# Optimization experiments

Measured on AMD Instinct MI355X. Metric: run time of the kernel, lower is better.

## Reference

```python
import jax, jax.numpy as jnp
import numpy as np

N_SAMPLE = 32
BETA = 1.0


def setup_inputs() -> dict:
    key = jax.random.key(0)
    k1, k2 = jax.random.split(key)
    # small scales so the gaussian kernel over 512 dims does not underflow
    x = jax.random.normal(k1, (2048, 512), dtype=jnp.float32) * 0.05
    W = jax.random.normal(k2, (512, 2048), dtype=jnp.float32) * 0.02  # Dense kernel [in, hidden]
    return {"x": x, "W": W}


def reference(x, W):
    B, H = x.shape[0], W.shape[1]
    # Encoder: h = x W ; z = softmax(h * beita)
    h = x @ W                                   # [B, H]
    z = jax.nn.softmax(h * BETA, axis=-1)       # [B, H]
    # Sampler: tf.random.categorical treats z (probs) as LOGITS -> same here.
    key = jax.random.key(42)
    # tf gives [B, n_sample]; jax categorical with shape=(NS, B) then .T matches that,
    # and the original code then RESHAPES (not transposes) to [NS, B] -> replicate scramble.
    samp = jax.random.categorical(key, z, axis=-1, shape=(N_SAMPLE, B)).T  # [B, NS]
    samp = samp.reshape(N_SAMPLE, B)            # faithful reshape, not transpose
    onehot = jax.nn.one_hot(samp, H, dtype=x.dtype)          # [NS, B, H]
    # tensordot(onehot, W, axes=[2,1]) -> gather rows of W^T as dense matmul
    x_decoded = jnp.einsum('nbh,dh->nbd', onehot, W)          # [NS, B, D]
    # gauss(x[None], x_decoded), var=1
    diff = x[None, :, :] - x_decoded                          # [NS, B, D]
    coeff = 1.0 / jnp.sqrt(2.0 * jnp.pi)
    temp = coeff * jnp.exp(-0.5 * jnp.sum(diff * diff, axis=-1))  # [NS, B]
    weight = temp / jnp.mean(temp, axis=0)                    # broadcast over NS
    return (h, z, onehot, x_decoded, weight)
```

## Files before the change

### kernel.cpp

```cpp
#include <hip/hip_runtime.h>
#include <stdint.h>
#include <math.h>

static constexpr int BDIM = 2048;
static constexpr int HDIM = 2048;
static constexpr int DDIM = 512;
static constexpr int NSAMP = 32;

static constexpr size_t OFF_H  = 0;
static constexpr size_t OFF_Z  = (size_t)BDIM * HDIM;
static constexpr size_t OFF_OH = OFF_Z + (size_t)BDIM * HDIM;
static constexpr size_t OFF_XD = OFF_OH + (size_t)NSAMP * BDIM * HDIM;
static constexpr size_t OFF_W  = OFF_XD + (size_t)NSAMP * BDIM * DDIM;

static constexpr size_t WS_WT    = 0;
static constexpr size_t WS_XB    = 1048576;
static constexpr size_t WS_WTB   = WS_XB + 524288;
static constexpr size_t WS_TEMP  = WS_WTB + 524288;
static constexpr size_t WS_DELTA = WS_TEMP + 65536;

typedef __attribute__((ext_vector_type(8))) short short8;
typedef __attribute__((ext_vector_type(4))) float f32x4;

__device__ __forceinline__ ushort f2bf(float f) {
  uint32_t x = __float_as_uint(f);
  return (ushort)((x + 0x7FFFu + ((x >> 16) & 1u)) >> 16);
}

__global__ __launch_bounds__(256) void cast_x_kernel(const float* __restrict__ x,
                                                     ushort* __restrict__ xb) {
  const int i = (blockIdx.x * 256 + threadIdx.x) * 4;
  float4 v = *(const float4*)(x + i);
  ushort4 o = {f2bf(v.x), f2bf(v.y), f2bf(v.z), f2bf(v.w)};
  *(ushort4*)(xb + i) = o;
}

__global__ __launch_bounds__(256) void transpose_kernel(const float* __restrict__ W,
                                                        float* __restrict__ Wt,
                                                        ushort* __restrict__ Wtb) {
  __shared__ float tile[32][33];
  const int tx = threadIdx.x & 31, ty = threadIdx.x >> 5;
  const int bx = blockIdx.x;
  const int by = blockIdx.y;
#pragma unroll
  for (int i = 0; i < 32; i += 8)
    tile[ty + i][tx] = W[(size_t)(by * 32 + ty + i) * HDIM + bx * 32 + tx];
  __syncthreads();
#pragma unroll
  for (int i = 0; i < 32; i += 8) {
    float v = tile[tx][ty + i];
    const size_t o = (size_t)(bx * 32 + ty + i) * DDIM + by * 32 + tx;
    Wt[o] = v;
    Wtb[o] = f2bf(v);
  }
}

__global__ __launch_bounds__(256) void gemm_mfma_kernel(const ushort* __restrict__ xb,
                                                        const ushort* __restrict__ wtb,
                                                        float* __restrict__ h) {
  __shared__ short As[128][72];
  __shared__ short Bs[128][72];
  const int tid = threadIdx.x;
  const int bm = blockIdx.y * 128, bn = blockIdx.x * 128;
  const int wave = tid >> 6, lane = tid & 63;
  const int wm = (wave >> 1) * 64, wn = (wave & 1) * 64;
  const int lrow = lane & 15, lk = (lane >> 4) * 8;

  f32x4 acc[4][4] = {};

  const int srow = tid >> 3;
  const int scol = (tid & 7) * 8;

  for (int k0 = 0; k0 < DDIM; k0 += 64) {
#pragma unroll
    for (int p = 0; p < 4; ++p) {
      const int r = srow + p * 32;
      short8 av = *(const short8*)(xb + (size_t)(bm + r) * DDIM + k0 + scol);
      short8 bv = *(const short8*)(wtb + (size_t)(bn + r) * DDIM + k0 + scol);
      *(short8*)&As[r][scol] = av;
      *(short8*)&Bs[r][scol] = bv;
    }
    __syncthreads();
#pragma unroll
    for (int kk = 0; kk < 64; kk += 32) {
      short8 af[4], bf[4];
#pragma unroll
      for (int i = 0; i < 4; ++i) {
        af[i] = *(const short8*)&As[wm + i * 16 + lrow][kk + lk];
        bf[i] = *(const short8*)&Bs[wn + i * 16 + lrow][kk + lk];
      }
#pragma unroll
      for (int i = 0; i < 4; ++i)
#pragma unroll
        for (int j = 0; j < 4; ++j)
          acc[i][j] = __builtin_amdgcn_mfma_f32_16x16x32_bf16(af[i], bf[j], acc[i][j], 0, 0, 0);
    }
    __syncthreads();
  }
#pragma unroll
  for (int i = 0; i < 4; ++i)
#pragma unroll
    for (int j = 0; j < 4; ++j)
#pragma unroll
      for (int rg = 0; rg < 4; ++rg) {
        const int row = bm + wm + i * 16 + (lane >> 4) * 4 + rg;
        const int col = bn + wn + j * 16 + (lane & 15);
        h[(size_t)row * HDIM + col] = acc[i][j][rg];
      }
}

__global__ __launch_bounds__(256) void softmax_kernel(const float* __restrict__ h,
                                                      float* __restrict__ z,
                                                      float* __restrict__ rowDelta) {
  const int b = blockIdx.x;
  const int tid = threadIdx.x;
  const int lane = tid & 63, wav = tid >> 6;
  const float* row = h + (size_t)b * HDIM;
  float* zrow = z + (size_t)b * HDIM;
  __shared__ float wmaxs[4], wmins[4], wsums[4];

  float vals[8];
  float vmax = -INFINITY, vmin = INFINITY;
#pragma unroll
  for (int k = 0; k < 8; ++k) {
    float v = row[tid + (k << 8)];
    vals[k] = v;
    vmax = fmaxf(vmax, v);
    vmin = fminf(vmin, v);
  }
#pragma unroll
  for (int off = 32; off > 0; off >>= 1) {
    vmax = fmaxf(vmax, __shfl_xor(vmax, off, 64));
    vmin = fminf(vmin, __shfl_xor(vmin, off, 64));
  }
  if (lane == 0) { wmaxs[wav] = vmax; wmins[wav] = vmin; }
  __syncthreads();
  const float rmax = fmaxf(fmaxf(wmaxs[0], wmaxs[1]), fmaxf(wmaxs[2], wmaxs[3]));
  const float rmin = fminf(fminf(wmins[0], wmins[1]), fminf(wmins[2], wmins[3]));

  float e[8];
  float lsum = 0.f;
#pragma unroll
  for (int k = 0; k < 8; ++k) {
    e[k] = expf(vals[k] - rmax);
    lsum += e[k];
  }
#pragma unroll
  for (int off = 32; off > 0; off >>= 1) lsum += __shfl_xor(lsum, off, 64);
  if (lane == 0) wsums[wav] = lsum;
  __syncthreads();
  const float rsum = wsums[0] + wsums[1] + wsums[2] + wsums[3];
#pragma unroll
  for (int k = 0; k < 8; ++k) zrow[tid + (k << 8)] = e[k] / rsum;
  if (tid == 0) rowDelta[b] = (1.0f - expf(rmin - rmax)) / rsum;
}

__device__ __forceinline__ void threefry_0_42(uint32_t x0, uint32_t x1,
                                              uint32_t& o0, uint32_t& o1) {
  const uint32_t ks0 = 0u, ks1 = 42u, ks2 = 0x1BD11BDAu ^ 0u ^ 42u;
  x0 += ks0; x1 += ks1;
#define TF_R(r) { x0 += x1; x1 = (x1 << (r)) | (x1 >> (32 - (r))); x1 ^= x0; }
  TF_R(13) TF_R(15) TF_R(26) TF_R(6)   x0 += ks1; x1 += ks2 + 1u;
  TF_R(17) TF_R(29) TF_R(16) TF_R(24)  x0 += ks2; x1 += ks0 + 2u;
  TF_R(13) TF_R(15) TF_R(26) TF_R(6)   x0 += ks0; x1 += ks1 + 3u;
  TF_R(17) TF_R(29) TF_R(16) TF_R(24)  x0 += ks1; x1 += ks2 + 4u;
  TF_R(13) TF_R(15) TF_R(26) TF_R(6)   x0 += ks2; x1 += ks0 + 5u;
#undef TF_R
  o0 = x0; o1 = x1;
}

__device__ __forceinline__ float bits_to_u(uint32_t bits) {
  float f = __uint_as_float((bits >> 9) | 0x3f800000u) - 1.0f;
  return (f == 0.0f) ? 1.1754943508222875e-38f : f;
}

__global__ __launch_bounds__(256) void sample_fused_kernel(
    const float* __restrict__ z, const float* __restrict__ rowDelta,
    const float* __restrict__ x, const float* __restrict__ Wt,
    float* __restrict__ oh, float* __restrict__ xd, float* __restrict__ temp) {
  const int wav = threadIdx.x >> 6;
  const int lane = threadIdx.x & 63;
  const int r = blockIdx.x * 4 + wav;
  const int b = r & (BDIM - 1);
  const float* zrow = z + (size_t)b * HDIM;

  const uint32_t base = (uint32_t)r << 11;
  uint32_t bb[32];
  uint32_t m23 = 0u;
#pragma unroll
  for (int k = 0; k < 32; ++k) {
    uint32_t o0, o1;
    threefry_0_42(0u, base + (uint32_t)(lane + (k << 6)), o0, o1);
    bb[k] = (o0 ^ o1) >> 9;
    m23 = max(m23, bb[k]);
  }
#pragma unroll
  for (int off = 32; off > 0; off >>= 1)
    m23 = max(m23, (uint32_t)__shfl_xor((int)m23, off, 64));
  const float umax = bits_to_u(m23 << 9);

  const float dpad = rowDelta[b] + 3e-4f;
  float uthr = expf(-expf(-(-logf(-logf(umax)) - dpad)));
  uthr = __uint_as_float(__float_as_uint(uthr) - 4u);
  uint32_t thr23 = __float_as_uint(1.0f + uthr) & 0x7FFFFFu;
  if (thr23 > 0u) thr23 -= 1u;

  double best = -1e300; int bh = 0x7fffffff;
#pragma unroll
  for (int k = 0; k < 32; ++k) {
    if (bb[k] >= thr23 || bb[k] == m23) {
      const int hh = lane + (k << 6);
      const float uk = bits_to_u(bb[k] << 9);
      double s = -log(-log((double)uk)) + (double)zrow[hh];
      if (s > best || (s == best && hh < bh)) { best = s; bh = hh; }
    }
  }
#pragma unroll
  for (int off = 32; off > 0; off >>= 1) {
    double so = __shfl_xor(best, off, 64);
    int ho = __shfl_xor(bh, off, 64);
    if (so > best || (so == best && ho < bh)) { best = so; bh = ho; }
  }

  const int j = ((r & (BDIM - 1)) << 5) | (r >> 11);
  const int c = j & (BDIM - 1);

  float* ohrow = oh + (size_t)j * HDIM;
#pragma unroll
  for (int k = 0; k < 8; ++k) {
    const int idx4 = (k << 6) + lane;
    const unsigned d = (unsigned)(bh - (idx4 << 2));
    float4 v;
    v.x = (d == 0u) ? 1.f : 0.f;
    v.y = (d == 1u) ? 1.f : 0.f;
    v.z = (d == 2u) ? 1.f : 0.f;
    v.w = (d == 3u) ? 1.f : 0.f;
    ((float4*)ohrow)[idx4] = v;
  }

  const float4* wrow = (const float4*)(Wt + (size_t)bh * DDIM);
  const float4* xrow = (const float4*)(x + (size_t)c * DDIM);
  float4* xdrow = (float4*)(xd + (size_t)j * DDIM);
  float ss = 0.f;
#pragma unroll
  for (int k = 0; k < 2; ++k) {
    const int idx4 = (k << 6) + lane;
    const float4 wv = wrow[idx4];
    const float4 xv = xrow[idx4];
    xdrow[idx4] = wv;
    const float dx = xv.x - wv.x, dy = xv.y - wv.y;
    const float dz = xv.z - wv.z, dw = xv.w - wv.w;
    ss += dx * dx + dy * dy + dz * dz + dw * dw;
  }
#pragma unroll
  for (int off = 32; off > 0; off >>= 1) ss += __shfl_xor(ss, off, 64);
  if (lane == 0) temp[j] = 0.3989422804014327f * expf(-0.5f * ss);
}

__global__ __launch_bounds__(256) void weight_kernel(const float* __restrict__ temp,
                                                     float* __restrict__ wout) {
  const int c = blockIdx.x * 256 + threadIdx.x;
  if (c >= BDIM) return;
  float sum = 0.f;
#pragma unroll
  for (int a = 0; a < NSAMP; ++a) sum += temp[a * BDIM + c];
  const float mean = sum / 32.0f;
#pragma unroll
  for (int a = 0; a < NSAMP; ++a) wout[a * BDIM + c] = temp[a * BDIM + c] / mean;
}

extern "C" void kernel_launch(void* const* d_in, const int* in_sizes, int n_in,
                              void* d_out, int out_size, void* d_ws, size_t ws_size,
                              hipStream_t stream) {
  (void)in_sizes; (void)n_in; (void)out_size; (void)ws_size;
  const float* x = (const float*)d_in[0];
  const float* W = (const float*)d_in[1];
  float* out = (float*)d_out;

  float* h  = out + OFF_H;
  float* z  = out + OFF_Z;
  float* oh = out + OFF_OH;
  float* xd = out + OFF_XD;
  float* wo = out + OFF_W;

  float* ws = (float*)d_ws;
  float* Wt = ws + WS_WT;
  ushort* xb = (ushort*)(ws + WS_XB);
  ushort* Wtb = (ushort*)(ws + WS_WTB);
  float* temp = ws + WS_TEMP;
  float* rowDelta = ws + WS_DELTA;

  cast_x_kernel<<<1024, 256, 0, stream>>>(x, xb);
  transpose_kernel<<<dim3(64, 16), 256, 0, stream>>>(W, Wt, Wtb);
  gemm_mfma_kernel<<<dim3(16, 16), 256, 0, stream>>>(xb, Wtb, h);
  softmax_kernel<<<2048, 256, 0, stream>>>(h, z, rowDelta);
  sample_fused_kernel<<<16384, 256, 0, stream>>>(z, rowDelta, x, Wt, oh, xd, temp);
  weight_kernel<<<8, 256, 0, stream>>>(temp, wo);
}
```

Baseline: 871.4 us.

## Merge prep kernels, vectorize softmax, nontemporal stores and early loads in sampler

```diff
diff --git a/kernel.cpp b/kernel.cpp
--- a/kernel.cpp
+++ b/kernel.cpp
@@ -27,21 +27,22 @@
   return (ushort)((x + 0x7FFFu + ((x >> 16) & 1u)) >> 16);
 }
 
-__global__ __launch_bounds__(256) void cast_x_kernel(const float* __restrict__ x,
-                                                     ushort* __restrict__ xb) {
-  const int i = (blockIdx.x * 256 + threadIdx.x) * 4;
-  float4 v = *(const float4*)(x + i);
-  ushort4 o = {f2bf(v.x), f2bf(v.y), f2bf(v.z), f2bf(v.w)};
-  *(ushort4*)(xb + i) = o;
-}
-
-__global__ __launch_bounds__(256) void transpose_kernel(const float* __restrict__ W,
-                                                        float* __restrict__ Wt,
-                                                        ushort* __restrict__ Wtb) {
+__global__ __launch_bounds__(256) void prep_kernel(const float* __restrict__ x,
+                                                   ushort* __restrict__ xb,
+                                                   const float* __restrict__ W,
+                                                   float* __restrict__ Wt,
+                                                   ushort* __restrict__ Wtb) {
   __shared__ float tile[32][33];
+  if (blockIdx.x >= 1024) {
+    const int i = ((blockIdx.x - 1024) * 256 + threadIdx.x) * 4;
+    float4 v = *(const float4*)(x + i);
+    ushort4 o = {f2bf(v.x), f2bf(v.y), f2bf(v.z), f2bf(v.w)};
+    *(ushort4*)(xb + i) = o;
+    return;
+  }
   const int tx = threadIdx.x & 31, ty = threadIdx.x >> 5;
-  const int bx = blockIdx.x;
-  const int by = blockIdx.y;
+  const int bx = blockIdx.x & 63;
+  const int by = blockIdx.x >> 6;
 #pragma unroll
   for (int i = 0; i < 32; i += 8)
     tile[ty + i][tx] = W[(size_t)(by * 32 + ty + i) * HDIM + bx * 32 + tx];
@@ -119,14 +120,14 @@
   float* zrow = z + (size_t)b * HDIM;
   __shared__ float wmaxs[4], wmins[4], wsums[4];
 
-  float vals[8];
+  const float4 v0 = ((const float4*)row)[tid * 2];
+  const float4 v1 = ((const float4*)row)[tid * 2 + 1];
+  float vals[8] = {v0.x, v0.y, v0.z, v0.w, v1.x, v1.y, v1.z, v1.w};
   float vmax = -INFINITY, vmin = INFINITY;
 #pragma unroll
   for (int k = 0; k < 8; ++k) {
-    float v = row[tid + (k << 8)];
-    vals[k] = v;
-    vmax = fmaxf(vmax, v);
-    vmin = fminf(vmin, v);
+    vmax = fmaxf(vmax, vals[k]);
+    vmin = fminf(vmin, vals[k]);
   }
 #pragma unroll
   for (int off = 32; off > 0; off >>= 1) {
@@ -150,8 +151,11 @@
   if (lane == 0) wsums[wav] = lsum;
   __syncthreads();
   const float rsum = wsums[0] + wsums[1] + wsums[2] + wsums[3];
-#pragma unroll
-  for (int k = 0; k < 8; ++k) zrow[tid + (k << 8)] = e[k] / rsum;
+  const float rinv = 1.0f / rsum;
+  float4 o0 = {e[0] * rinv, e[1] * rinv, e[2] * rinv, e[3] * rinv};
+  float4 o1 = {e[4] * rinv, e[5] * rinv, e[6] * rinv, e[7] * rinv};
+  ((float4*)zrow)[tid * 2] = o0;
+  ((float4*)zrow)[tid * 2 + 1] = o1;
   if (tid == 0) rowDelta[b] = (1.0f - expf(rmin - rmax)) / rsum;
 }
 
@@ -174,7 +178,7 @@
   return (f == 0.0f) ? 1.1754943508222875e-38f : f;
 }
 
-__global__ __launch_bounds__(256) void sample_fused_kernel(
+__global__ __launch_bounds__(256, 4) void sample_fused_kernel(
     const float* __restrict__ z, const float* __restrict__ rowDelta,
     const float* __restrict__ x, const float* __restrict__ Wt,
     float* __restrict__ oh, float* __restrict__ xd, float* __restrict__ temp) {
@@ -184,6 +188,13 @@
   const int b = r & (BDIM - 1);
   const float* zrow = z + (size_t)b * HDIM;
 
+  const int j = ((r & (BDIM - 1)) << 5) | (r >> 11);
+  const int c = j & (BDIM - 1);
+  const f32x4* xrow = (const f32x4*)(x + (size_t)c * DDIM);
+  const f32x4 xv0 = xrow[lane];
+  const f32x4 xv1 = xrow[64 + lane];
+  const float dpad0 = rowDelta[b];
+
   const uint32_t base = (uint32_t)r << 11;
   uint32_t bb[32];
   uint32_t m23 = 0u;
@@ -199,7 +210,7 @@
     m23 = max(m23, (uint32_t)__shfl_xor((int)m23, off, 64));
   const float umax = bits_to_u(m23 << 9);
 
-  const float dpad = rowDelta[b] + 3e-4f;
+  const float dpad = dpad0 + 3e-4f;
   float uthr = expf(-expf(-(-logf(-logf(umax)) - dpad)));
   uthr = __uint_as_float(__float_as_uint(uthr) - 4u);
   uint32_t thr23 = __float_as_uint(1.0f + uthr) & 0x7FFFFFu;
@@ -222,34 +233,34 @@
     if (so > best || (so == best && ho < bh)) { best = so; bh = ho; }
   }
 
-  const int j = ((r & (BDIM - 1)) << 5) | (r >> 11);
-  const int c = j & (BDIM - 1);
-
-  float* ohrow = oh + (size_t)j * HDIM;
+  f32x4* ohrow = (f32x4*)(oh + (size_t)j * HDIM);
 #pragma unroll
   for (int k = 0; k < 8; ++k) {
     const int idx4 = (k << 6) + lane;
     const unsigned d = (unsigned)(bh - (idx4 << 2));
-    float4 v;
+    f32x4 v;
     v.x = (d == 0u) ? 1.f : 0.f;
     v.y = (d == 1u) ? 1.f : 0.f;
     v.z = (d == 2u) ? 1.f : 0.f;
     v.w = (d == 3u) ? 1.f : 0.f;
-    ((float4*)ohrow)[idx4] = v;
-  }
-
-  const float4* wrow = (const float4*)(Wt + (size_t)bh * DDIM);
-  const float4* xrow = (const float4*)(x + (size_t)c * DDIM);
-  float4* xdrow = (float4*)(xd + (size_t)j * DDIM);
+    __builtin_nontemporal_store(v, &ohrow[idx4]);
+  }
+
+  const f32x4* wrow = (const f32x4*)(Wt + (size_t)bh * DDIM);
+  f32x4* xdrow = (f32x4*)(xd + (size_t)j * DDIM);
+  const f32x4 wv0 = wrow[lane];
+  const f32x4 wv1 = wrow[64 + lane];
+  __builtin_nontemporal_store(wv0, &xdrow[lane]);
+  __builtin_nontemporal_store(wv1, &xdrow[64 + lane]);
   float ss = 0.f;
-#pragma unroll
-  for (int k = 0; k < 2; ++k) {
-    const int idx4 = (k << 6) + lane;
-    const float4 wv = wrow[idx4];
-    const float4 xv = xrow[idx4];
-    xdrow[idx4] = wv;
-    const float dx = xv.x - wv.x, dy = xv.y - wv.y;
-    const float dz = xv.z - wv.z, dw = xv.w - wv.w;
+  {
+    const float dx = xv0.x - wv0.x, dy = xv0.y - wv0.y;
+    const float dz = xv0.z - wv0.z, dw = xv0.w - wv0.w;
+    ss += dx * dx + dy * dy + dz * dz + dw * dw;
+  }
+  {
+    const float dx = xv1.x - wv1.x, dy = xv1.y - wv1.y;
+    const float dz = xv1.z - wv1.z, dw = xv1.w - wv1.w;
     ss += dx * dx + dy * dy + dz * dz + dw * dw;
   }
 #pragma unroll
@@ -290,8 +301,7 @@
   float* temp = ws + WS_TEMP;
   float* rowDelta = ws + WS_DELTA;
 
-  cast_x_kernel<<<1024, 256, 0, stream>>>(x, xb);
-  transpose_kernel<<<dim3(64, 16), 256, 0, stream>>>(W, Wt, Wtb);
+  prep_kernel<<<2048, 256, 0, stream>>>(x, xb, W, Wt, Wtb);
   gemm_mfma_kernel<<<dim3(16, 16), 256, 0, stream>>>(xb, Wtb, h);
   softmax_kernel<<<2048, 256, 0, stream>>>(h, z, rowDelta);
   sample_fused_kernel<<<16384, 256, 0, stream>>>(z, rowDelta, x, Wt, oh, xd, temp);
```

New measurement: 860.4 us. About the same (-1.3%).
